# Optimization experiments

Hardware: AMD Instinct MI355X
Metric: run time of the kernel (lower is better)

The kernel has to match this reference:

```python
import jax, jax.numpy as jnp
import numpy as np


def _sample_choices(prob_weights, key):
    # softmax over edge-type dim, take P(NORMAL_EDGE)=index 1
    prob_edge = jax.nn.softmax(prob_weights, axis=-1)[..., 1]  # [out, in]
    k_bern, k_fix = jax.random.split(key)
    choices = jax.random.bernoulli(k_bern, prob_edge).astype(prob_weights.dtype)  # [out, in]
    # zero-connection fixup: rows with no sampled edge get one random connection
    out_f, in_f = choices.shape
    conn_count = jnp.sum(choices, axis=-1)  # [out]
    rand_cols = jax.random.randint(k_fix, (out_f,), 0, in_f)  # [out]
    fix = ((conn_count == 0)[:, None] & (jnp.arange(in_f)[None, :] == rand_cols[:, None]))
    choices = choices + fix.astype(choices.dtype)
    # selected edges -> 0, unselected -> 1 (min operator branch; no *-1 negation)
    mask = jnp.abs(choices - 1.0)
    return mask


def reference(x, prob_weights):
    # x: [B, in], prob_weights: [out, in, 2]
    mask = _sample_choices(prob_weights, jax.random.key(42))  # [out, in]
    # result[b, o] = min_i (x[b, i] + mask[o, i])  -- [B, out, in] intermediate
    operator_inputs = x[:, None, :] + mask[None, :, :]
    return jnp.min(operator_inputs, axis=-1)  # [B, out]


def setup_inputs() -> dict:
    key = jax.random.key(0)
    k_x, k_w = jax.random.split(key)
    B, IN, OUT = 512, 512, 512
    x = jax.random.uniform(k_x, (B, IN), dtype=jnp.float32)
    prob_weights = jax.random.uniform(k_w, (OUT, IN, 2), dtype=jnp.float32)
    return {"x": x, "prob_weights": prob_weights}
```

## Files before the change

kernel.cpp:

```cpp
#include <hip/hip_runtime.h>
#include <cstdint>

#define JAX_PARTITIONABLE 1

__host__ __device__ inline void threefry2x32(uint32_t k0, uint32_t k1,
                                             uint32_t x0, uint32_t x1,
                                             uint32_t& o0, uint32_t& o1) {
  const uint32_t ks2 = k0 ^ k1 ^ 0x1BD11BDAu;
  uint32_t v0 = x0 + k0, v1 = x1 + k1;
#define RL(v, r) (((v) << (r)) | ((v) >> (32 - (r))))
#define RND4(a, b, c, d)                                                       \
  v0 += v1; v1 = RL(v1, a); v1 ^= v0;                                          \
  v0 += v1; v1 = RL(v1, b); v1 ^= v0;                                          \
  v0 += v1; v1 = RL(v1, c); v1 ^= v0;                                          \
  v0 += v1; v1 = RL(v1, d); v1 ^= v0;
  RND4(13, 15, 26, 6)  v0 += k1;  v1 += ks2 + 1u;
  RND4(17, 29, 16, 24) v0 += ks2; v1 += k0 + 2u;
  RND4(13, 15, 26, 6)  v0 += k0;  v1 += k1 + 3u;
  RND4(17, 29, 16, 24) v0 += k1;  v1 += ks2 + 4u;
  RND4(13, 15, 26, 6)  v0 += ks2; v1 += k0 + 5u;
#undef RND4
#undef RL
  o0 = v0; o1 = v1;
}

#define IN_F 512
#define OUT_F 512
#define BATCH 512

__global__ __launch_bounds__(512) void gen_mask_kernel(
    const float* __restrict__ pw, float* __restrict__ M,
    uint32_t kb0, uint32_t kb1, uint32_t kl0, uint32_t kl1) {
  const int o = blockIdx.x;
  const int i = threadIdx.x;

  const float2 w = ((const float2*)pw)[o * IN_F + i];
  const float mx = fmaxf(w.x, w.y);
  const float e0 = expf(w.x - mx);
  const float e1 = expf(w.y - mx);
  const float p = e1 / (e0 + e1);

  const uint32_t n = (uint32_t)(o * IN_F + i);
  uint32_t h0, h1, bits;
#if JAX_PARTITIONABLE
  threefry2x32(kb0, kb1, 0u, n, h0, h1);
  bits = h0 ^ h1;
#else
  {
    const uint32_t half = (uint32_t)(OUT_F * IN_F / 2);
    if (n < half) { threefry2x32(kb0, kb1, n, n + half, h0, h1); bits = h0; }
    else          { threefry2x32(kb0, kb1, n - half, n, h0, h1); bits = h1; }
  }
#endif
  const float u = __uint_as_float((bits >> 9) | 0x3F800000u) - 1.0f;
  const bool c = u < p;

  __shared__ unsigned long long words[8];
  __shared__ int cnt;
  if (i == 0) cnt = 0;
  __syncthreads();
  const unsigned long long bal = __ballot(c);
  if ((i & 63) == 0) {
    words[i >> 6] = bal;
    atomicAdd(&cnt, __popcll(bal));
  }
  __syncthreads();
  if (cnt == 0 && i == 0) {
    uint32_t c0, c1, rb;
#if JAX_PARTITIONABLE
    threefry2x32(kl0, kl1, 0u, (uint32_t)o, c0, c1);
    rb = c0 ^ c1;
#else
    if (o < 256) { threefry2x32(kl0, kl1, (uint32_t)o, (uint32_t)(o + 256), c0, c1); rb = c0; }
    else         { threefry2x32(kl0, kl1, (uint32_t)(o - 256), (uint32_t)o, c0, c1); rb = c1; }
#endif
    const uint32_t col = rb & (IN_F - 1);
    words[col >> 6] |= (1ull << (col & 63u));
  }
  __syncthreads();
  const bool sel = (words[i >> 6] >> (i & 63)) & 1ull;
  M[o * IN_F + i] = sel ? 0.0f : 1e9f;
}

#define BT 64
#define OT 32
#define KT 64
#define NZ 2

__global__ __launch_bounds__(256) void minplus_kernel(
    const float* __restrict__ x, const float* __restrict__ M,
    float* __restrict__ part) {
  __shared__ __align__(16) float xs[KT][BT + 4];
  __shared__ __align__(16) float ms[KT][OT + 4];

  const int tid = threadIdx.x;
  const int tx = tid & 15;
  const int ty = tid >> 4;
  const int b0 = blockIdx.x * BT;
  const int o0 = blockIdx.y * OT;
  const int z = blockIdx.z;
  const int kbeg = z * (IN_F / NZ);

  float acc[4][2];
#pragma unroll
  for (int p = 0; p < 4; ++p) { acc[p][0] = 1e30f; acc[p][1] = 1e30f; }

  const int lr = tid >> 4;
  const int lc = (tid & 15) * 4;

  for (int kt = 0; kt < IN_F / NZ; kt += KT) {
    const int kk = kbeg + kt;
#pragma unroll
    for (int j = 0; j < 4; ++j) {
      const int r = j * 16 + lr;
      const float4 v = *(const float4*)&x[(b0 + r) * IN_F + kk + lc];
      xs[lc + 0][r] = v.x; xs[lc + 1][r] = v.y;
      xs[lc + 2][r] = v.z; xs[lc + 3][r] = v.w;
    }
#pragma unroll
    for (int j = 0; j < 2; ++j) {
      const int r = j * 16 + lr;
      const float4 v = *(const float4*)&M[(o0 + r) * IN_F + kk + lc];
      ms[lc + 0][r] = v.x; ms[lc + 1][r] = v.y;
      ms[lc + 2][r] = v.z; ms[lc + 3][r] = v.w;
    }
    __syncthreads();
#pragma unroll
    for (int k = 0; k < KT; ++k) {
      const float4 xv = *(const float4*)&xs[k][tx * 4];
      const float2 mv = *(const float2*)&ms[k][ty * 2];
      acc[0][0] = fminf(acc[0][0], xv.x + mv.x);
      acc[1][0] = fminf(acc[1][0], xv.y + mv.x);
      acc[2][0] = fminf(acc[2][0], xv.z + mv.x);
      acc[3][0] = fminf(acc[3][0], xv.w + mv.x);
      acc[0][1] = fminf(acc[0][1], xv.x + mv.y);
      acc[1][1] = fminf(acc[1][1], xv.y + mv.y);
      acc[2][1] = fminf(acc[2][1], xv.z + mv.y);
      acc[3][1] = fminf(acc[3][1], xv.w + mv.y);
    }
    __syncthreads();
  }

  float* pz = part + (size_t)z * (BATCH * OUT_F);
#pragma unroll
  for (int p = 0; p < 4; ++p) {
    const float2 st = make_float2(acc[p][0], acc[p][1]);
    *(float2*)&pz[(b0 + tx * 4 + p) * OUT_F + o0 + ty * 2] = st;
  }
}

__global__ __launch_bounds__(256) void reduce_kernel(
    const float* __restrict__ part, float* __restrict__ out) {
  const int n = blockIdx.x * 256 + threadIdx.x;
  const float4 a = ((const float4*)part)[n];
  const float4 b = ((const float4*)(part + BATCH * OUT_F))[n];
  ((float4*)out)[n] = make_float4(fminf(a.x, b.x), fminf(a.y, b.y),
                                  fminf(a.z, b.z), fminf(a.w, b.w));
}

extern "C" void kernel_launch(void* const* d_in, const int* in_sizes, int n_in,
                              void* d_out, int out_size, void* d_ws, size_t ws_size,
                              hipStream_t stream) {
  (void)in_sizes; (void)n_in; (void)out_size; (void)ws_size;
  const float* x = (const float*)d_in[0];
  const float* pw = (const float*)d_in[1];
  float* M = (float*)d_ws;
  float* part = (float*)d_ws + BATCH * OUT_F;
  float* out = (float*)d_out;

  uint32_t kb0, kb1, kf0, kf1, kl0, kl1;
#if JAX_PARTITIONABLE
  threefry2x32(0u, 42u, 0u, 0u, kb0, kb1);
  threefry2x32(0u, 42u, 0u, 1u, kf0, kf1);
  threefry2x32(kf0, kf1, 0u, 1u, kl0, kl1);
#else
  uint32_t a0, a1, b0_, b1_, c0, c1, d0, d1;
  threefry2x32(0u, 42u, 0u, 2u, a0, a1);
  threefry2x32(0u, 42u, 1u, 3u, b0_, b1_);
  kb0 = a0; kb1 = b0_;
  kf0 = a1; kf1 = b1_;
  threefry2x32(kf0, kf1, 0u, 2u, c0, c1);
  threefry2x32(kf0, kf1, 1u, 3u, d0, d1);
  kl0 = c1; kl1 = d1;
#endif

  gen_mask_kernel<<<dim3(OUT_F), dim3(IN_F), 0, stream>>>(pw, M, kb0, kb1, kl0, kl1);
  minplus_kernel<<<dim3(BATCH / BT, OUT_F / OT, NZ), dim3(256), 0, stream>>>(x, M, part);
  reduce_kernel<<<dim3(BATCH * OUT_F / 4 / 256), dim3(256), 0, stream>>>(part, out);
}
```

Before: 79.87 us.

## Drop split-K reduction and use smaller per-thread tiles writing output directly

Removes the two-way K split and its separate reduce kernel, so the min-plus kernel walks the full inner dimension and writes the final output directly. Block tiles shrink to 32x16 with KT=128, and each thread now holds 2 accumulators instead of 8, which raises the block count and occupancy. The cost is much lower register-level reuse: more shared-memory loads per min/add, with padded shared arrays and scalar strided output stores. It also deletes the unused non-partitionable RNG path.

Measured after the change: 75.31 us. 1.06x faster.

```diff
diff --git a/kernel.cpp b/kernel.cpp
--- a/kernel.cpp
+++ b/kernel.cpp
@@ -1,7 +1,5 @@
 #include <hip/hip_runtime.h>
 #include <cstdint>
-
-#define JAX_PARTITIONABLE 1
 
 __host__ __device__ inline void threefry2x32(uint32_t k0, uint32_t k1,
                                              uint32_t x0, uint32_t x1,
@@ -41,17 +39,9 @@
   const float p = e1 / (e0 + e1);
 
   const uint32_t n = (uint32_t)(o * IN_F + i);
-  uint32_t h0, h1, bits;
-#if JAX_PARTITIONABLE
+  uint32_t h0, h1;
   threefry2x32(kb0, kb1, 0u, n, h0, h1);
-  bits = h0 ^ h1;
-#else
-  {
-    const uint32_t half = (uint32_t)(OUT_F * IN_F / 2);
-    if (n < half) { threefry2x32(kb0, kb1, n, n + half, h0, h1); bits = h0; }
-    else          { threefry2x32(kb0, kb1, n - half, n, h0, h1); bits = h1; }
-  }
-#endif
+  const uint32_t bits = h0 ^ h1;
   const float u = __uint_as_float((bits >> 9) | 0x3F800000u) - 1.0f;
   const bool c = u < p;
 
@@ -66,14 +56,9 @@
   }
   __syncthreads();
   if (cnt == 0 && i == 0) {
-    uint32_t c0, c1, rb;
-#if JAX_PARTITIONABLE
+    uint32_t c0, c1;
     threefry2x32(kl0, kl1, 0u, (uint32_t)o, c0, c1);
-    rb = c0 ^ c1;
-#else
-    if (o < 256) { threefry2x32(kl0, kl1, (uint32_t)o, (uint32_t)(o + 256), c0, c1); rb = c0; }
-    else         { threefry2x32(kl0, kl1, (uint32_t)(o - 256), (uint32_t)o, c0, c1); rb = c1; }
-#endif
+    const uint32_t rb = c0 ^ c1;
     const uint32_t col = rb & (IN_F - 1);
     words[col >> 6] |= (1ull << (col & 63u));
   }
@@ -82,80 +67,55 @@
   M[o * IN_F + i] = sel ? 0.0f : 1e9f;
 }
 
-#define BT 64
-#define OT 32
-#define KT 64
-#define NZ 2
+#define BT 32
+#define OT 16
+#define KT 128
 
 __global__ __launch_bounds__(256) void minplus_kernel(
     const float* __restrict__ x, const float* __restrict__ M,
-    float* __restrict__ part) {
-  __shared__ __align__(16) float xs[KT][BT + 4];
-  __shared__ __align__(16) float ms[KT][OT + 4];
+    float* __restrict__ out) {
+  __shared__ float xs[KT][BT + 1];
+  __shared__ float ms[KT][OT + 1];
 
   const int tid = threadIdx.x;
   const int tx = tid & 15;
   const int ty = tid >> 4;
   const int b0 = blockIdx.x * BT;
   const int o0 = blockIdx.y * OT;
-  const int z = blockIdx.z;
-  const int kbeg = z * (IN_F / NZ);
 
-  float acc[4][2];
-#pragma unroll
-  for (int p = 0; p < 4; ++p) { acc[p][0] = 1e30f; acc[p][1] = 1e30f; }
+  const int sr = tid >> 5;
+  const int sc = (tid & 31) * 4;
 
-  const int lr = tid >> 4;
-  const int lc = (tid & 15) * 4;
+  float acc0 = 1e30f, acc1 = 1e30f;
 
-  for (int kt = 0; kt < IN_F / NZ; kt += KT) {
-    const int kk = kbeg + kt;
+  for (int kt = 0; kt < IN_F; kt += KT) {
 #pragma unroll
     for (int j = 0; j < 4; ++j) {
-      const int r = j * 16 + lr;
-      const float4 v = *(const float4*)&x[(b0 + r) * IN_F + kk + lc];
-      xs[lc + 0][r] = v.x; xs[lc + 1][r] = v.y;
-      xs[lc + 2][r] = v.z; xs[lc + 3][r] = v.w;
+      const int r = j * 8 + sr;
+      const float4 v = *(const float4*)&x[(b0 + r) * IN_F + kt + sc];
+      xs[sc + 0][r] = v.x; xs[sc + 1][r] = v.y;
+      xs[sc + 2][r] = v.z; xs[sc + 3][r] = v.w;
     }
 #pragma unroll
     for (int j = 0; j < 2; ++j) {
-      const int r = j * 16 + lr;
-      const float4 v = *(const float4*)&M[(o0 + r) * IN_F + kk + lc];
-      ms[lc + 0][r] = v.x; ms[lc + 1][r] = v.y;
-      ms[lc + 2][r] = v.z; ms[lc + 3][r] = v.w;
+      const int r = j * 8 + sr;
+      const float4 v = *(const float4*)&M[(o0 + r) * IN_F + kt + sc];
+      ms[sc + 0][r] = v.x; ms[sc + 1][r] = v.y;
+      ms[sc + 2][r] = v.z; ms[sc + 3][r] = v.w;
     }
     __syncthreads();
-#pragma unroll
+#pragma unroll 16
     for (int k = 0; k < KT; ++k) {
-      const float4 xv = *(const float4*)&xs[k][tx * 4];
-      const float2 mv = *(const float2*)&ms[k][ty * 2];
-      acc[0][0] = fminf(acc[0][0], xv.x + mv.x);
-      acc[1][0] = fminf(acc[1][0], xv.y + mv.x);
-      acc[2][0] = fminf(acc[2][0], xv.z + mv.x);
-      acc[3][0] = fminf(acc[3][0], xv.w + mv.x);
-      acc[0][1] = fminf(acc[0][1], xv.x + mv.y);
-      acc[1][1] = fminf(acc[1][1], xv.y + mv.y);
-      acc[2][1] = fminf(acc[2][1], xv.z + mv.y);
-      acc[3][1] = fminf(acc[3][1], xv.w + mv.y);
+      const float2 xv = *(const float2*)&xs[k][tx * 2];
+      const float mv = ms[k][ty];
+      acc0 = fminf(acc0, xv.x + mv);
+      acc1 = fminf(acc1, xv.y + mv);
     }
     __syncthreads();
   }
 
-  float* pz = part + (size_t)z * (BATCH * OUT_F);
-#pragma unroll
-  for (int p = 0; p < 4; ++p) {
-    const float2 st = make_float2(acc[p][0], acc[p][1]);
-    *(float2*)&pz[(b0 + tx * 4 + p) * OUT_F + o0 + ty * 2] = st;
-  }
-}
-
-__global__ __launch_bounds__(256) void reduce_kernel(
-    const float* __restrict__ part, float* __restrict__ out) {
-  const int n = blockIdx.x * 256 + threadIdx.x;
-  const float4 a = ((const float4*)part)[n];
-  const float4 b = ((const float4*)(part + BATCH * OUT_F))[n];
-  ((float4*)out)[n] = make_float4(fminf(a.x, b.x), fminf(a.y, b.y),
-                                  fminf(a.z, b.z), fminf(a.w, b.w));
+  out[(b0 + tx * 2 + 0) * OUT_F + o0 + ty] = acc0;
+  out[(b0 + tx * 2 + 1) * OUT_F + o0 + ty] = acc1;
 }
 
 extern "C" void kernel_launch(void* const* d_in, const int* in_sizes, int n_in,
@@ -165,26 +125,13 @@
   const float* x = (const float*)d_in[0];
   const float* pw = (const float*)d_in[1];
   float* M = (float*)d_ws;
-  float* part = (float*)d_ws + BATCH * OUT_F;
   float* out = (float*)d_out;
 
   uint32_t kb0, kb1, kf0, kf1, kl0, kl1;
-#if JAX_PARTITIONABLE
   threefry2x32(0u, 42u, 0u, 0u, kb0, kb1);
   threefry2x32(0u, 42u, 0u, 1u, kf0, kf1);
   threefry2x32(kf0, kf1, 0u, 1u, kl0, kl1);
-#else
-  uint32_t a0, a1, b0_, b1_, c0, c1, d0, d1;
-  threefry2x32(0u, 42u, 0u, 2u, a0, a1);
-  threefry2x32(0u, 42u, 1u, 3u, b0_, b1_);
-  kb0 = a0; kb1 = b0_;
-  kf0 = a1; kf1 = b1_;
-  threefry2x32(kf0, kf1, 0u, 2u, c0, c1);
-  threefry2x32(kf0, kf1, 1u, 3u, d0, d1);
-  kl0 = c1; kl1 = d1;
-#endif
 
   gen_mask_kernel<<<dim3(OUT_F), dim3(IN_F), 0, stream>>>(pw, M, kb0, kb1, kl0, kl1);
-  minplus_kernel<<<dim3(BATCH / BT, OUT_F / OT, NZ), dim3(256), 0, stream>>>(x, M, part);
-  reduce_kernel<<<dim3(BATCH * OUT_F / 4 / 256), dim3(256), 0, stream>>>(part, out);
+  minplus_kernel<<<dim3(BATCH / BT, OUT_F / OT), dim3(256), 0, stream>>>(x, M, out);
 }
```
